# Kernel tuning notes

Hardware: AMD Instinct MI355X
Metric: run time of the kernel (lower is better)

Reference implementation:

```python
import jax, jax.numpy as jnp
import numpy as np

HIDDEN = 1024
NUM_HEADS = 16
HEAD_DIM = HIDDEN // NUM_HEADS
ROPE_THETA = 10000.0


def rope_tables(seq_len, head_dim, theta):
    inv_freq = 1.0 / theta ** (jnp.arange(0, head_dim, 2, dtype=jnp.float32) / head_dim)
    pos = jnp.arange(seq_len, dtype=jnp.float32)
    freqs = jnp.outer(pos, inv_freq)  # [S, hd/2]
    return jnp.cos(freqs), jnp.sin(freqs)


def apply_rope(x, cos, sin):
    # x: [B, nh, S, hd]; cos/sin: [S, hd/2]
    x1, x2 = jnp.split(x, 2, axis=-1)
    return jnp.concatenate([x1 * cos - x2 * sin, x2 * cos + x1 * sin], axis=-1)


def setup_inputs() -> dict:
    key = jax.random.key(0)
    k1, k2, k3 = jax.random.split(key, 3)
    B, S = 2, 2048
    hidden_states = jax.random.normal(k1, (B, S, HIDDEN), dtype=jnp.float32)
    # nn.Linear stores weight as [out, in]; y = x @ W.T
    Wqkv = jax.random.normal(k2, (3 * HIDDEN, HIDDEN), dtype=jnp.float32) * (HIDDEN ** -0.5)
    Wo = jax.random.normal(k3, (HIDDEN, HIDDEN), dtype=jnp.float32) * (HIDDEN ** -0.5)
    return {"hidden_states": hidden_states, "Wqkv": Wqkv, "Wo": Wo}


def reference(hidden_states, Wqkv, Wo):
    B, S, H = hidden_states.shape
    qkv = hidden_states @ Wqkv.T  # [B, S, 3H]
    qkv = qkv.reshape(B, S, 3, NUM_HEADS, HEAD_DIM)
    q, k, v = jnp.moveaxis(qkv, 2, 0)  # each [B, S, nh, hd]
    q = jnp.transpose(q, (0, 2, 1, 3))  # [B, nh, S, hd]
    k = jnp.transpose(k, (0, 2, 1, 3))
    v = jnp.transpose(v, (0, 2, 1, 3))
    cos, sin = rope_tables(S, HEAD_DIM, ROPE_THETA)
    q = apply_rope(q, cos, sin)
    k = apply_rope(k, cos, sin)
    scale = 1.0 / jnp.sqrt(jnp.asarray(HEAD_DIM, dtype=q.dtype))
    scores = jnp.einsum("bhqd,bhkd->bhqk", q, k) * scale
    causal = jnp.tril(jnp.ones((S, S), dtype=bool))
    scores = jnp.where(causal, scores, jnp.finfo(scores.dtype).min)
    attn = jax.nn.softmax(scores, axis=-1)
    out = jnp.einsum("bhqk,bhkd->bhqd", attn, v)  # [B, nh, S, hd]
    out = jnp.transpose(out, (0, 2, 1, 3)).reshape(B, S, H)
    return out @ Wo.T
```

## Files before the change

kernel.cpp:

```cpp
#include <hip/hip_runtime.h>
#include <hip/hip_bf16.h>
#include <math.h>

typedef __bf16 bf16_t;
typedef __attribute__((ext_vector_type(8))) __bf16 bf16x8;
typedef __attribute__((ext_vector_type(4))) float f32x4;
typedef __attribute__((ext_vector_type(16))) float f32x16;
typedef __attribute__((ext_vector_type(4))) unsigned u32x4;

#define AS1(p) ((__attribute__((address_space(1))) void*)(p))
#define AS3(p) ((__attribute__((address_space(3))) void*)(p))

__device__ inline unsigned pkbf(float a, float b) {
  bf16_t x = (bf16_t)a, y = (bf16_t)b;
  return (unsigned)__builtin_bit_cast(unsigned short, x) |
         ((unsigned)__builtin_bit_cast(unsigned short, y) << 16);
}
__device__ inline f32x16 zero16() {
  f32x16 z;
#pragma unroll
  for (int r = 0; r < 16; ++r) z[r] = 0.f;
  return z;
}

__device__ inline void cvt8(const float* __restrict__ in, bf16_t* __restrict__ out, int i) {
  const float4* p = (const float4*)in;
  float4 a = p[2 * i], b = p[2 * i + 1];
  bf16x8 o;
  o[0] = (bf16_t)a.x; o[1] = (bf16_t)a.y; o[2] = (bf16_t)a.z; o[3] = (bf16_t)a.w;
  o[4] = (bf16_t)b.x; o[5] = (bf16_t)b.y; o[6] = (bf16_t)b.z; o[7] = (bf16_t)b.w;
  ((bf16x8*)out)[i] = o;
}

__global__ __launch_bounds__(256)
void prep_all(const float* __restrict__ hid, const float* __restrict__ wqkv,
              const float* __restrict__ wo, bf16_t* __restrict__ hidb,
              bf16_t* __restrict__ wqkvb, bf16_t* __restrict__ wob,
              float* __restrict__ cosb, float* __restrict__ sinb) {
  const int bid = blockIdx.x, tid = threadIdx.x;
  if (bid < 2048) {
    cvt8(hid, hidb, bid * 256 + tid);
  } else if (bid < 3584) {
    cvt8(wqkv, wqkvb, (bid - 2048) * 256 + tid);
  } else if (bid < 4096) {
    cvt8(wo, wob, (bid - 3584) * 256 + tid);
  } else {
    int t = (bid - 4096) * 256 + tid;
    int s = t >> 5, i = t & 31;
    float inv = powf(10000.0f, -(float)i / 32.0f);
    float sv, cv;
    sincosf((float)s * inv, &sv, &cv);
    cosb[t] = cv;
    sinb[t] = sv;
  }
}

__global__ __launch_bounds__(256, 2)
void gemm_qkv(const bf16_t* __restrict__ A, const bf16_t* __restrict__ B,
              bf16_t* __restrict__ qkv, bf16_t* __restrict__ Kp,
              const float* __restrict__ cosb, const float* __restrict__ sinb) {
  __shared__ __align__(16) bf16_t lA[2][128 * 64];
  __shared__ __align__(16) bf16_t lB[2][128 * 64];
  const int K = 1024;
  const int tid = threadIdx.x;
  const int wid = tid >> 6, lane = tid & 63;
  const int lr = lane & 15, lg = lane >> 4;
  const int nwg = gridDim.x * gridDim.y;
  int lin = blockIdx.y * gridDim.x + blockIdx.x;
  lin = (lin & 7) * (nwg >> 3) + (lin >> 3);
  const int m0 = (lin / gridDim.x) * 128, n0 = (lin % gridDim.x) * 128;
  const int wm = (wid >> 1) * 64, wn = (wid & 1) * 64;
  const int srow = lane >> 3;
  const int scol = (lane & 7) * 8;
  f32x4 acc[4][4];
#pragma unroll
  for (int i = 0; i < 4; ++i)
#pragma unroll
    for (int j = 0; j < 4; ++j) acc[i][j] = f32x4{0.f, 0.f, 0.f, 0.f};

#define GSTAGE(KT, BUF)                                                                    \
  do {                                                                                     \
    const int k0_ = (KT) << 6;                                                             \
    _Pragma("unroll")                                                                      \
    for (int i_ = 0; i_ < 4; ++i_) {                                                       \
      int c_ = (wid << 2) + i_;                                                            \
      int r_ = (c_ << 3) + srow;                                                           \
      __builtin_amdgcn_global_load_lds(AS1(A + (size_t)(m0 + r_) * K + k0_ + scol),        \
                                       AS3(&lA[BUF][c_ * 512]), 16, 0, 0);                 \
      __builtin_amdgcn_global_load_lds(AS1(B + (size_t)(n0 + r_) * K + k0_ + scol),        \
                                       AS3(&lB[BUF][c_ * 512]), 16, 0, 0);                 \
    }                                                                                      \
  } while (0)

  GSTAGE(0, 0);
  for (int kt = 0; kt < 16; ++kt) {
    const int buf = kt & 1;
    if (kt < 15) {
      GSTAGE(kt + 1, buf ^ 1);
      asm volatile("s_waitcnt vmcnt(8)" ::: "memory");
    } else {
      asm volatile("s_waitcnt vmcnt(0)" ::: "memory");
    }
    __builtin_amdgcn_s_barrier();
#pragma unroll
    for (int ks = 0; ks < 2; ++ks) {
      bf16x8 af[4], bfr[4];
#pragma unroll
      for (int i = 0; i < 4; ++i) {
        af[i]  = *(const bf16x8*)&lA[buf][(wm + i * 16 + lr) * 64 + ks * 32 + lg * 8];
        bfr[i] = *(const bf16x8*)&lB[buf][(wn + i * 16 + lr) * 64 + ks * 32 + lg * 8];
      }
#pragma unroll
      for (int i = 0; i < 4; ++i)
#pragma unroll
        for (int j = 0; j < 4; ++j)
          acc[i][j] = __builtin_amdgcn_mfma_f32_16x16x32_bf16(af[i], bfr[j], acc[i][j], 0, 0, 0);
    }
    __builtin_amdgcn_s_barrier();
  }
#undef GSTAGE
  const int sec = n0 >> 10;
  const int hcol = ((n0 + wn) & 1023) >> 6;
  if (sec == 2) {
#pragma unroll
    for (int i = 0; i < 4; ++i) {
      int token0 = m0 + wm + i * 16 + lg * 4;
      int bb = token0 >> 11;
      int t = (token0 & 2047) >> 6;
      int kv0 = token0 & 63;
      bf16_t* vd = qkv + ((size_t)(bb * 2048 + t * 64)) * 3072 + 2048 + hcol * 64;
#pragma unroll
      for (int j = 0; j < 4; ++j) {
        int d = j * 16 + lr;
        uint2 w;
        w.x = pkbf(acc[i][j][0], acc[i][j][1]);
        w.y = pkbf(acc[i][j][2], acc[i][j][3]);
        *(uint2*)(vd + (size_t)d * 3072 + (((kv0 >> 3) ^ (d & 7)) * 8) + (kv0 & 7)) = w;
      }
    }
  } else {
    const float SC = sec ? 1.0f : 0.125f * 1.4426950408889634f;
#pragma unroll
    for (int i = 0; i < 4; ++i)
#pragma unroll
      for (int r = 0; r < 4; ++r) {
        int token = m0 + wm + i * 16 + lg * 4 + r;
        int s = token & 2047;
#pragma unroll
        for (int j = 0; j < 2; ++j) {
          int f = j * 16 + lr;
          float cv = cosb[s * 32 + f], sv = sinb[s * 32 + f];
          float x1 = acc[i][j][r], x2 = acc[i][j + 2][r];
          float y1 = (x1 * cv - x2 * sv) * SC;
          float y2 = (x2 * cv + x1 * sv) * SC;
          if (sec == 0) {
            bf16_t* qd = qkv + (size_t)token * 3072 + hcol * 64;
            qd[f] = (bf16_t)y1;
            qd[f + 32] = (bf16_t)y2;
          } else {
            int bb = token >> 11, t = (token & 2047) >> 6, rk = token & 63;
            bf16_t* kd = Kp + ((size_t)((bb * 16 + hcol) * 32 + t)) * 4096 + rk * 64;
            int c1 = f >> 3;
            kd[((c1 ^ (rk & 7)) * 8) + (lr & 7)] = (bf16_t)y1;
            kd[(((c1 + 4) ^ (rk & 7)) * 8) + (lr & 7)] = (bf16_t)y2;
          }
        }
      }
  }
}

__global__ __launch_bounds__(256, 2)
void gemm_nt_f32(const bf16_t* __restrict__ A, const bf16_t* __restrict__ B,
                 float* __restrict__ C, int M, int N, int K) {
  __shared__ __align__(16) bf16_t lA[2][128 * 64];
  __shared__ __align__(16) bf16_t lB[2][128 * 64];
  const int tid = threadIdx.x;
  const int wid = tid >> 6, lane = tid & 63;
  const int lr = lane & 15, lg = lane >> 4;
  const int nwg = gridDim.x * gridDim.y;
  int lin = blockIdx.y * gridDim.x + blockIdx.x;
  lin = (lin & 7) * (nwg >> 3) + (lin >> 3);
  const int m0 = (lin / gridDim.x) * 128, n0 = (lin % gridDim.x) * 128;
  const int wm = (wid >> 1) * 64, wn = (wid & 1) * 64;
  const int srow = lane >> 3;
  const int scol = (lane & 7) * 8;
  f32x4 acc[4][4];
#pragma unroll
  for (int i = 0; i < 4; ++i)
#pragma unroll
    for (int j = 0; j < 4; ++j) acc[i][j] = f32x4{0.f, 0.f, 0.f, 0.f};

#define GSTAGE(KT, BUF)                                                                    \
  do {                                                                                     \
    const int k0_ = (KT) << 6;                                                             \
    _Pragma("unroll")                                                                      \
    for (int i_ = 0; i_ < 4; ++i_) {                                                       \
      int c_ = (wid << 2) + i_;                                                            \
      int r_ = (c_ << 3) + srow;                                                           \
      __builtin_amdgcn_global_load_lds(AS1(A + (size_t)(m0 + r_) * K + k0_ + scol),        \
                                       AS3(&lA[BUF][c_ * 512]), 16, 0, 0);                 \
      __builtin_amdgcn_global_load_lds(AS1(B + (size_t)(n0 + r_) * K + k0_ + scol),        \
                                       AS3(&lB[BUF][c_ * 512]), 16, 0, 0);                 \
    }                                                                                      \
  } while (0)

  const int nk = K >> 6;
  GSTAGE(0, 0);
  for (int kt = 0; kt < nk; ++kt) {
    const int buf = kt & 1;
    if (kt + 1 < nk) {
      GSTAGE(kt + 1, buf ^ 1);
      asm volatile("s_waitcnt vmcnt(8)" ::: "memory");
    } else {
      asm volatile("s_waitcnt vmcnt(0)" ::: "memory");
    }
    __builtin_amdgcn_s_barrier();
#pragma unroll
    for (int ks = 0; ks < 2; ++ks) {
      bf16x8 af[4], bfr[4];
#pragma unroll
      for (int i = 0; i < 4; ++i) {
        af[i]  = *(const bf16x8*)&lA[buf][(wm + i * 16 + lr) * 64 + ks * 32 + lg * 8];
        bfr[i] = *(const bf16x8*)&lB[buf][(wn + i * 16 + lr) * 64 + ks * 32 + lg * 8];
      }
#pragma unroll
      for (int i = 0; i < 4; ++i)
#pragma unroll
        for (int j = 0; j < 4; ++j)
          acc[i][j] = __builtin_amdgcn_mfma_f32_16x16x32_bf16(af[i], bfr[j], acc[i][j], 0, 0, 0);
    }
    __builtin_amdgcn_s_barrier();
  }
#undef GSTAGE
#pragma unroll
  for (int i = 0; i < 4; ++i)
#pragma unroll
    for (int j = 0; j < 4; ++j)
#pragma unroll
      for (int r = 0; r < 4; ++r) {
        int row = m0 + wm + i * 16 + lg * 4 + r;
        int col = n0 + wn + j * 16 + lr;
        C[(size_t)row * N + col] = acc[i][j][r];
      }
}

__device__ const unsigned char ROLE_LUT[44] = {
    19, 18, 17, 16,
    15, 95, 159, 158,
    14, 94, 93, 157,
    13, 92, 156, 91, 155, 154,
    12, 90, 89, 153, 152,
    11, 88, 87, 151, 150,
    10, 86, 85, 149, 148,
    9, 84,
    8, 7, 6, 5, 4, 3, 2, 1, 0};

__global__ __launch_bounds__(128, 2)
void attn_fwd(const bf16_t* __restrict__ qkv, const bf16_t* __restrict__ Kp,
              bf16_t* __restrict__ O, bf16_t* __restrict__ Po, float* __restrict__ Plp) {
  __shared__ __align__(16) bf16_t Ksh[2][4096];
  __shared__ __align__(16) bf16_t Vsh[2][4096];
  const int tid = threadIdx.x, wid = tid >> 6, lane = tid & 63;
  const int ln = lane & 31, h = lane >> 5;
  const int lin = blockIdx.x;
  const int e = ROLE_LUT[lin >> 5];
  const int bh = lin & 31;
  const int c = e & 31, kind = e >> 6;
  const int b = bh >> 4, hd = bh & 15;
  const int t0 = (kind == 2) ? ((c + 1) >> 1) : 0;
  const int t1 = (kind == 1) ? ((c + 1) >> 1) : c + 1;
  const int qw = c * 64 + wid * 32;

  const bf16_t* Qrow = qkv + ((size_t)(b * 2048 + qw + ln)) * 3072 + hd * 64;
  bf16x8 qf[4];
#pragma unroll
  for (int t = 0; t < 4; ++t) qf[t] = *(const bf16x8*)(Qrow + t * 16 + h * 8);

  f32x16 o0 = zero16(), o1 = zero16();
  float lp = 0.f;

  const bf16_t* Kbase = Kp + ((size_t)bh * 32) * 4096 + tid * 8;
  const bf16_t* Vbase = qkv + ((size_t)(b * 2048 + (tid >> 3))) * 3072 + 2048 + hd * 64 + (tid & 7) * 8;

#define STAGE(T, BUF)                                                                     \
  do {                                                                                    \
    const bf16_t* ks = Kbase + (size_t)(T) * 4096;                                        \
    __builtin_amdgcn_global_load_lds(AS1(ks),        AS3(&Ksh[BUF][tid * 8]), 16, 0, 0);  \
    __builtin_amdgcn_global_load_lds(AS1(ks + 1024), AS3(&Ksh[BUF][1024 + tid * 8]), 16, 0, 0); \
    __builtin_amdgcn_global_load_lds(AS1(ks + 2048), AS3(&Ksh[BUF][2048 + tid * 8]), 16, 0, 0); \
    __builtin_amdgcn_global_load_lds(AS1(ks + 3072), AS3(&Ksh[BUF][3072 + tid * 8]), 16, 0, 0); \
    const bf16_t* vs = Vbase + (size_t)(T) * 64 * 3072;                                   \
    __builtin_amdgcn_global_load_lds(AS1(vs),             AS3(&Vsh[BUF][tid * 8]), 16, 0, 0);        \
    __builtin_amdgcn_global_load_lds(AS1(vs + 16 * 3072), AS3(&Vsh[BUF][1024 + tid * 8]), 16, 0, 0); \
    __builtin_amdgcn_global_load_lds(AS1(vs + 32 * 3072), AS3(&Vsh[BUF][2048 + tid * 8]), 16, 0, 0); \
    __builtin_amdgcn_global_load_lds(AS1(vs + 48 * 3072), AS3(&Vsh[BUF][3072 + tid * 8]), 16, 0, 0); \
  } while (0)

  STAGE(t0, t0 & 1);
  for (int t = t0; t < t1; ++t) {
    asm volatile("s_waitcnt vmcnt(0)" ::: "memory");
    __builtin_amdgcn_s_barrier();
    if (t + 1 < t1) STAGE(t + 1, (t + 1) & 1);
    const bf16_t* K = &Ksh[t & 1][0];
    const bf16_t* V = &Vsh[t & 1][0];
    f32x16 s0 = zero16(), s1 = zero16();
    __builtin_amdgcn_s_setprio(1);
#pragma unroll
    for (int u = 0; u < 4; ++u) {
      const int ch = 2 * u + h;
      bf16x8 k0 = *(const bf16x8*)&K[ln * 64 + ((ch ^ (ln & 7)) * 8)];
      bf16x8 k1 = *(const bf16x8*)&K[(32 + ln) * 64 + ((ch ^ (ln & 7)) * 8)];
      s0 = __builtin_amdgcn_mfma_f32_32x32x16_bf16(k0, qf[u], s0, 0, 0, 0);
      s1 = __builtin_amdgcn_mfma_f32_32x32x16_bf16(k1, qf[u], s1, 0, 0, 0);
    }
    __builtin_amdgcn_s_setprio(0);
    if (t == c) {
      const int qg = qw + ln, k0g = t * 64;
#pragma unroll
      for (int r = 0; r < 16; ++r) {
        int kv = k0g + (r & 3) + 8 * (r >> 2) + 4 * h;
        if (kv > qg) s0[r] = -3e38f;
        if (kv + 32 > qg) s1[r] = -3e38f;
      }
    }
#pragma unroll
    for (int r = 0; r < 16; ++r) {
      float p0 = __builtin_amdgcn_exp2f(s0[r]); lp += p0; s0[r] = p0;
      float p1 = __builtin_amdgcn_exp2f(s1[r]); lp += p1; s1[r] = p1;
    }
    __builtin_amdgcn_s_setprio(1);
#pragma unroll
    for (int u = 0; u < 4; ++u) {
      const int w = u & 1;
      f32x16 sv = (u >> 1) ? s1 : s0;
      unsigned x  = pkbf(sv[8 * w + 0], sv[8 * w + 1]);
      unsigned x2 = pkbf(sv[8 * w + 2], sv[8 * w + 3]);
      unsigned y  = pkbf(sv[8 * w + 4], sv[8 * w + 5]);
      unsigned y2 = pkbf(sv[8 * w + 6], sv[8 * w + 7]);
      asm volatile("v_permlane32_swap_b32 %0, %1" : "+v"(x), "+v"(y));
      asm volatile("v_permlane32_swap_b32 %0, %1" : "+v"(x2), "+v"(y2));
      u32x4 pw; pw[0] = x; pw[1] = x2; pw[2] = y; pw[3] = y2;
      bf16x8 pf = __builtin_bit_cast(bf16x8, pw);
      const int ch = 2 * u + h;
      bf16x8 v0 = *(const bf16x8*)&V[ln * 64 + ((ch ^ (ln & 7)) * 8)];
      bf16x8 v1 = *(const bf16x8*)&V[(32 + ln) * 64 + ((ch ^ (ln & 7)) * 8)];
      o0 = __builtin_amdgcn_mfma_f32_32x32x16_bf16(v0, pf, o0, 0, 0, 0);
      o1 = __builtin_amdgcn_mfma_f32_32x32x16_bf16(v1, pf, o1, 0, 0, 0);
    }
    __builtin_amdgcn_s_setprio(0);
  }
#undef STAGE
  float lpf = lp + __shfl_xor(lp, 32, 64);
  if (kind == 0) {
    float inv = 1.0f / lpf;
    bf16_t* Oaddr = O + ((size_t)(b * 2048 + qw + ln)) * 1024 + hd * 64;
#pragma unroll
    for (int D = 0; D < 2; ++D) {
      f32x16 ov = D ? o1 : o0;
#pragma unroll
      for (int Q = 0; Q < 4; ++Q) {
        uint2 w;
        w.x = pkbf(ov[4 * Q + 0] * inv, ov[4 * Q + 1] * inv);
        w.y = pkbf(ov[4 * Q + 2] * inv, ov[4 * Q + 3] * inv);
        *(uint2*)(Oaddr + D * 32 + Q * 8 + 4 * h) = w;
      }
    }
  } else {
    const int slot = (bh * 12 + (c - 20)) * 2 + (kind - 1);
    const int qi = wid * 32 + ln;
    if (h == 0) Plp[slot * 64 + qi] = lpf;
    bf16_t* Paddr = Po + ((size_t)(slot * 64 + qi)) * 64;
#pragma unroll
    for (int D = 0; D < 2; ++D) {
      f32x16 ov = D ? o1 : o0;
#pragma unroll
      for (int Q = 0; Q < 4; ++Q) {
        uint2 w;
        w.x = pkbf(ov[4 * Q + 0], ov[4 * Q + 1]);
        w.y = pkbf(ov[4 * Q + 2], ov[4 * Q + 3]);
        *(uint2*)(Paddr + D * 32 + Q * 8 + 4 * h) = w;
      }
    }
  }
}

__global__ __launch_bounds__(64)
void attn_combine(const bf16_t* __restrict__ Po, const float* __restrict__ Plp,
                  bf16_t* __restrict__ O) {
  const int blk = blockIdx.x;
  const int bh = blk / 12, sc = blk % 12;
  const int b = bh >> 4, hd = bh & 15;
  const int c = 20 + sc;
  const int q = threadIdx.x;
  const int slotA = (bh * 12 + sc) * 2, slotB = slotA + 1;
  float inv = 1.0f / (Plp[slotA * 64 + q] + Plp[slotB * 64 + q]);
  const bf16x8* pa = (const bf16x8*)(Po + ((size_t)(slotA * 64 + q)) * 64);
  const bf16x8* pb = (const bf16x8*)(Po + ((size_t)(slotB * 64 + q)) * 64);
  bf16_t* oaddr = O + ((size_t)(b * 2048 + c * 64 + q)) * 1024 + hd * 64;
#pragma unroll
  for (int j = 0; j < 8; ++j) {
    bf16x8 a = pa[j], v = pb[j];
    bf16x8 w;
#pragma unroll
    for (int k = 0; k < 8; ++k) w[k] = (bf16_t)(((float)a[k] + (float)v[k]) * inv);
    ((bf16x8*)oaddr)[j] = w;
  }
}

extern "C" void kernel_launch(void* const* d_in, const int* in_sizes, int n_in,
                              void* d_out, int out_size, void* d_ws, size_t ws_size,
                              hipStream_t stream) {
  const float* hid  = (const float*)d_in[0];
  const float* wqkv = (const float*)d_in[1];
  const float* wo   = (const float*)d_in[2];
  float* out = (float*)d_out;
  char* ws = (char*)d_ws;
  bf16_t* hidb  = (bf16_t*)(ws);
  bf16_t* wqkvb = (bf16_t*)(ws + 8388608);
  bf16_t* wob   = (bf16_t*)(ws + 14680064);
  bf16_t* qkvb  = (bf16_t*)(ws + 16777216);
  float*  cosb  = (float*)(ws + 41943040);
  float*  sinb  = (float*)(ws + 42205184);
  bf16_t* Ob    = (bf16_t*)(ws + 42467328);
  bf16_t* Kp    = (bf16_t*)(ws + 52428800);
  bf16_t* Po    = (bf16_t*)(ws + 60817408);
  float*  Plp   = (float*)(ws + 67108864);

  prep_all<<<4352, 256, 0, stream>>>(hid, wqkv, wo, hidb, wqkvb, wob, cosb, sinb);
  gemm_qkv<<<dim3(24, 32), 256, 0, stream>>>(hidb, wqkvb, qkvb, Kp, cosb, sinb);
  attn_fwd<<<1408, 128, 0, stream>>>(qkvb, Kp, Ob, Po, Plp);
  attn_combine<<<384, 64, 0, stream>>>(Po, Plp, Ob);
  gemm_nt_f32<<<dim3(8, 32), 256, 0, stream>>>(Ob, wob, out, 4096, 1024, 1024);
}
```

Baseline: 130.2 us.

## Triple-buffer GEMM K-tiles at BK=32 and raise occupancy to three blocks

```diff
diff --git a/kernel.cpp b/kernel.cpp
--- a/kernel.cpp
+++ b/kernel.cpp
@@ -55,12 +55,26 @@
   }
 }
 
-__global__ __launch_bounds__(256, 2)
+#define GSTAGE32(KT, BUF)                                                                  \
+  do {                                                                                     \
+    const int k0_ = (KT) << 5;                                                             \
+    const int ar_ = tid >> 2, ac_ = (tid & 3) * 8;                                         \
+    __builtin_amdgcn_global_load_lds(AS1(A + (size_t)(m0 + ar_) * K + k0_ + ac_),          \
+                                     AS3(&lA[BUF][ar_ * 32 + ac_]), 16, 0, 0);             \
+    __builtin_amdgcn_global_load_lds(AS1(A + (size_t)(m0 + 64 + ar_) * K + k0_ + ac_),     \
+                                     AS3(&lA[BUF][(64 + ar_) * 32 + ac_]), 16, 0, 0);      \
+    __builtin_amdgcn_global_load_lds(AS1(B + (size_t)(n0 + ar_) * K + k0_ + ac_),          \
+                                     AS3(&lB[BUF][ar_ * 32 + ac_]), 16, 0, 0);             \
+    __builtin_amdgcn_global_load_lds(AS1(B + (size_t)(n0 + 64 + ar_) * K + k0_ + ac_),     \
+                                     AS3(&lB[BUF][(64 + ar_) * 32 + ac_]), 16, 0, 0);      \
+  } while (0)
+
+__global__ __launch_bounds__(256, 3)
 void gemm_qkv(const bf16_t* __restrict__ A, const bf16_t* __restrict__ B,
               bf16_t* __restrict__ qkv, bf16_t* __restrict__ Kp,
               const float* __restrict__ cosb, const float* __restrict__ sinb) {
-  __shared__ __align__(16) bf16_t lA[2][128 * 64];
-  __shared__ __align__(16) bf16_t lB[2][128 * 64];
+  __shared__ __align__(16) bf16_t lA[3][128 * 32];
+  __shared__ __align__(16) bf16_t lB[3][128 * 32];
   const int K = 1024;
   const int tid = threadIdx.x;
   const int wid = tid >> 6, lane = tid & 63;
@@ -70,45 +84,33 @@
   lin = (lin & 7) * (nwg >> 3) + (lin >> 3);
   const int m0 = (lin / gridDim.x) * 128, n0 = (lin % gridDim.x) * 128;
   const int wm = (wid >> 1) * 64, wn = (wid & 1) * 64;
-  const int srow = lane >> 3;
-  const int scol = (lane & 7) * 8;
   f32x4 acc[4][4];
 #pragma unroll
   for (int i = 0; i < 4; ++i)
 #pragma unroll
     for (int j = 0; j < 4; ++j) acc[i][j] = f32x4{0.f, 0.f, 0.f, 0.f};
 
-#define GSTAGE(KT, BUF)                                                                    \
-  do {                                                                                     \
-    const int k0_ = (KT) << 6;                                                             \
-    _Pragma("unroll")                                                                      \
-    for (int i_ = 0; i_ < 4; ++i_) {                                                       \
-      int c_ = (wid << 2) + i_;                                                            \
-      int r_ = (c_ << 3) + srow;                                                           \
-      __builtin_amdgcn_global_load_lds(AS1(A + (size_t)(m0 + r_) * K + k0_ + scol),        \
-                                       AS3(&lA[BUF][c_ * 512]), 16, 0, 0);                 \
-      __builtin_amdgcn_global_load_lds(AS1(B + (size_t)(n0 + r_) * K + k0_ + scol),        \
-                                       AS3(&lB[BUF][c_ * 512]), 16, 0, 0);                 \
-    }                                                                                      \
-  } while (0)
-
-  GSTAGE(0, 0);
-  for (int kt = 0; kt < 16; ++kt) {
-    const int buf = kt & 1;
-    if (kt < 15) {
-      GSTAGE(kt + 1, buf ^ 1);
+  const int nk = 32;
+  GSTAGE32(0, 0);
+  GSTAGE32(1, 1);
+  int cbuf = 0;
+  for (int kt = 0; kt < nk; ++kt) {
+    if (kt + 2 < nk) {
+      const int sb = cbuf == 0 ? 2 : cbuf - 1;
+      GSTAGE32(kt + 2, sb);
       asm volatile("s_waitcnt vmcnt(8)" ::: "memory");
+    } else if (kt + 1 < nk) {
+      asm volatile("s_waitcnt vmcnt(4)" ::: "memory");
     } else {
       asm volatile("s_waitcnt vmcnt(0)" ::: "memory");
     }
     __builtin_amdgcn_s_barrier();
-#pragma unroll
-    for (int ks = 0; ks < 2; ++ks) {
+    {
       bf16x8 af[4], bfr[4];
 #pragma unroll
       for (int i = 0; i < 4; ++i) {
-        af[i]  = *(const bf16x8*)&lA[buf][(wm + i * 16 + lr) * 64 + ks * 32 + lg * 8];
-        bfr[i] = *(const bf16x8*)&lB[buf][(wn + i * 16 + lr) * 64 + ks * 32 + lg * 8];
+        af[i]  = *(const bf16x8*)&lA[cbuf][(wm + i * 16 + lr) * 32 + lg * 8];
+        bfr[i] = *(const bf16x8*)&lB[cbuf][(wn + i * 16 + lr) * 32 + lg * 8];
       }
 #pragma unroll
       for (int i = 0; i < 4; ++i)
@@ -117,8 +119,8 @@
           acc[i][j] = __builtin_amdgcn_mfma_f32_16x16x32_bf16(af[i], bfr[j], acc[i][j], 0, 0, 0);
     }
     __builtin_amdgcn_s_barrier();
-  }
-#undef GSTAGE
+    cbuf = cbuf == 2 ? 0 : cbuf + 1;
+  }
   const int sec = n0 >> 10;
   const int hcol = ((n0 + wn) & 1023) >> 6;
   if (sec == 2) {
@@ -169,11 +171,11 @@
   }
 }
 
-__global__ __launch_bounds__(256, 2)
+__global__ __launch_bounds__(256, 3)
 void gemm_nt_f32(const bf16_t* __restrict__ A, const bf16_t* __restrict__ B,
                  float* __restrict__ C, int M, int N, int K) {
-  __shared__ __align__(16) bf16_t lA[2][128 * 64];
-  __shared__ __align__(16) bf16_t lB[2][128 * 64];
+  __shared__ __align__(16) bf16_t lA[3][128 * 32];
+  __shared__ __align__(16) bf16_t lB[3][128 * 32];
   const int tid = threadIdx.x;
   const int wid = tid >> 6, lane = tid & 63;
   const int lr = lane & 15, lg = lane >> 4;
@@ -182,46 +184,33 @@
   lin = (lin & 7) * (nwg >> 3) + (lin >> 3);
   const int m0 = (lin / gridDim.x) * 128, n0 = (lin % gridDim.x) * 128;
   const int wm = (wid >> 1) * 64, wn = (wid & 1) * 64;
-  const int srow = lane >> 3;
-  const int scol = (lane & 7) * 8;
   f32x4 acc[4][4];
 #pragma unroll
   for (int i = 0; i < 4; ++i)
 #pragma unroll
     for (int j = 0; j < 4; ++j) acc[i][j] = f32x4{0.f, 0.f, 0.f, 0.f};
 
-#define GSTAGE(KT, BUF)                                                                    \
-  do {                                                                                     \
-    const int k0_ = (KT) << 6;                                                             \
-    _Pragma("unroll")                                                                      \
-    for (int i_ = 0; i_ < 4; ++i_) {                                                       \
-      int c_ = (wid << 2) + i_;                                                            \
-      int r_ = (c_ << 3) + srow;                                                           \
-      __builtin_amdgcn_global_load_lds(AS1(A + (size_t)(m0 + r_) * K + k0_ + scol),        \
-                                       AS3(&lA[BUF][c_ * 512]), 16, 0, 0);                 \
-      __builtin_amdgcn_global_load_lds(AS1(B + (size_t)(n0 + r_) * K + k0_ + scol),        \
-                                       AS3(&lB[BUF][c_ * 512]), 16, 0, 0);                 \
-    }                                                                                      \
-  } while (0)
-
-  const int nk = K >> 6;
-  GSTAGE(0, 0);
+  const int nk = K >> 5;
+  GSTAGE32(0, 0);
+  GSTAGE32(1, 1);
+  int cbuf = 0;
   for (int kt = 0; kt < nk; ++kt) {
-    const int buf = kt & 1;
-    if (kt + 1 < nk) {
-      GSTAGE(kt + 1, buf ^ 1);
+    if (kt + 2 < nk) {
+      const int sb = cbuf == 0 ? 2 : cbuf - 1;
+      GSTAGE32(kt + 2, sb);
       asm volatile("s_waitcnt vmcnt(8)" ::: "memory");
+    } else if (kt + 1 < nk) {
+      asm volatile("s_waitcnt vmcnt(4)" ::: "memory");
     } else {
       asm volatile("s_waitcnt vmcnt(0)" ::: "memory");
     }
     __builtin_amdgcn_s_barrier();
-#pragma unroll
-    for (int ks = 0; ks < 2; ++ks) {
+    {
       bf16x8 af[4], bfr[4];
 #pragma unroll
       for (int i = 0; i < 4; ++i) {
-        af[i]  = *(const bf16x8*)&lA[buf][(wm + i * 16 + lr) * 64 + ks * 32 + lg * 8];
-        bfr[i] = *(const bf16x8*)&lB[buf][(wn + i * 16 + lr) * 64 + ks * 32 + lg * 8];
+        af[i]  = *(const bf16x8*)&lA[cbuf][(wm + i * 16 + lr) * 32 + lg * 8];
+        bfr[i] = *(const bf16x8*)&lB[cbuf][(wn + i * 16 + lr) * 32 + lg * 8];
       }
 #pragma unroll
       for (int i = 0; i < 4; ++i)
@@ -230,8 +219,8 @@
           acc[i][j] = __builtin_amdgcn_mfma_f32_16x16x32_bf16(af[i], bfr[j], acc[i][j], 0, 0, 0);
     }
     __builtin_amdgcn_s_barrier();
-  }
-#undef GSTAGE
+    cbuf = cbuf == 2 ? 0 : cbuf + 1;
+  }
 #pragma unroll
   for (int i = 0; i < 4; ++i)
 #pragma unroll
```

New measurement: 114.5 us. 1.14x faster.
